# Performance work log

Hardware: AMD Instinct MI355X
Metric: run time of the kernel (lower is better)

The kernel has to match this reference:

```python
import jax, jax.numpy as jnp
import numpy as np

HIDDEN = 2048
FFN = 2048      # ffn_hidden_size (tp_size == 1)
E = 8           # moe_num_experts
TOP_K = 2       # moe_top_k
S = 2048        # number of tokens


def setup_inputs() -> dict:
    key = jax.random.key(0)
    k1, k2, k3, k4 = jax.random.split(key, 4)
    return {
        "hidden_states": jax.random.normal(k1, (S, HIDDEN), jnp.float32),
        "w_qkv": jax.random.normal(k2, (3 * E, HIDDEN), jnp.float32) * 0.02,
        "w1": jax.random.normal(k3, (E, HIDDEN, 2 * FFN), jnp.float32) * 0.02,
        "w2": jax.random.normal(k4, (E, FFN, HIDDEN), jnp.float32) * 0.02,
        "top_k": TOP_K,
    }


def reference(hidden_states, w_qkv, w1, w2, top_k):
    S, H = hidden_states.shape
    # --- ParallelAttention_router (gate), computed in fp32 as in the source ---
    mix = hidden_states @ w_qkv.T                                  # [S, 3E]
    q, k, v = jnp.split(mix.astype(jnp.float32), 3, axis=-1)       # each [S, E]
    # attn_weights[s,i,j] = q[s,i]*k[s,j]; softmax over j; logits = attn @ v
    attn = jax.nn.softmax(q[:, :, None] * k[:, None, :], axis=-1)  # [S, E, E]
    logits = jnp.einsum('sij,sj->si', attn, v)                     # [S, E]
    # --- top-k routing: softmax over selected logits ---
    top_logits, indices = jax.lax.top_k(logits, top_k)             # [S, K]
    scores = jax.nn.softmax(top_logits, axis=-1).astype(hidden_states.dtype)
    # --- experts: per-expert GLU MLP. The torch code sorts tokens by expert and
    # runs a grouped-GEMM loop; mathematically out[s] = sum_k scores[s,k] *
    # MLP_{indices[s,k]}(x[s]). We compute all experts densely (static shapes)
    # and gather/combine, which is the same math. ---
    fc1 = jnp.einsum('sh,ehi->esi', hidden_states, w1)             # [E, S, 2*FFN]
    g, u = jnp.split(fc1, 2, axis=-1)
    inter = jax.nn.silu(g) * u                                     # [E, S, FFN]
    expert_out = jnp.einsum('esi,eih->esh', inter, w2)             # [E, S, H]
    tok = jnp.arange(S)
    out = jnp.zeros_like(hidden_states)
    for kk in range(top_k):  # tiny static loop over top_k (=2)
        out = out + scores[:, kk, None] * expert_out[indices[:, kk], tok]
    return out
```

## Files before the change

kernel.cpp:

```cpp
#include <hip/hip_runtime.h>
#include <math.h>

#define S_TOK 2048
#define HID   2048
#define FFN_  2048
#define NEXP  8
#define NSLOT (S_TOK*2)

typedef short  s8v __attribute__((ext_vector_type(8)));
typedef short  s4v __attribute__((ext_vector_type(4)));
typedef float  f4v __attribute__((ext_vector_type(4)));

__device__ __forceinline__ unsigned short f32_bf16(float f){
  unsigned u = __float_as_uint(f);
  u += 0x7fffu + ((u>>16)&1u);
  return (unsigned short)(u>>16);
}
__device__ __forceinline__ int lds_off(int r,int kq){
  return (r*4 + (kq ^ ((r>>2)&3)))*8;
}

__global__ void init_k(int* hdr){
  if (threadIdx.x < 24) hdr[threadIdx.x] = 0;
}

__global__ __launch_bounds__(256) void convX_k(
    const float* __restrict__ X, unsigned short* __restrict__ Xb)
{
  int i = (blockIdx.x*256 + threadIdx.x)*8;
  f4v a = *reinterpret_cast<const f4v*>(X + i);
  f4v b = *reinterpret_cast<const f4v*>(X + i + 4);
  s8v o;
  o[0]=(short)f32_bf16(a[0]); o[1]=(short)f32_bf16(a[1]);
  o[2]=(short)f32_bf16(a[2]); o[3]=(short)f32_bf16(a[3]);
  o[4]=(short)f32_bf16(b[0]); o[5]=(short)f32_bf16(b[1]);
  o[6]=(short)f32_bf16(b[2]); o[7]=(short)f32_bf16(b[3]);
  *reinterpret_cast<s8v*>(Xb + i) = o;
}

__global__ __launch_bounds__(256) void transp_k(
    const float* __restrict__ src, unsigned short* __restrict__ dst,
    int K, int N)
{
  const int e = blockIdx.z;
  const int n0 = blockIdx.x*64, k0 = blockIdx.y*64;
  src += (size_t)e*K*N;
  dst += (size_t)e*N*K;
  __shared__ __align__(16) unsigned short t[64][72];
  const int tid = threadIdx.x;
  const int r = tid>>2, cq = tid&3;
  #pragma unroll
  for (int i=0;i<4;i++){
    f4v f = *reinterpret_cast<const f4v*>(src + (size_t)(k0+r)*N + n0 + cq*16 + i*4);
    #pragma unroll
    for (int j=0;j<4;j++) t[cq*16+i*4+j][r] = f32_bf16(f[j]);
  }
  __syncthreads();
  #pragma unroll
  for (int i=0;i<2;i++){
    s8v v = *reinterpret_cast<const s8v*>(&t[r][cq*16 + i*8]);
    *reinterpret_cast<s8v*>(dst + (size_t)(n0+r)*K + k0 + cq*16 + i*8) = v;
  }
}

__global__ __launch_bounds__(64) void router_k(
    const float* __restrict__ X, const float* __restrict__ Wqkv,
    int* __restrict__ hdr, int* __restrict__ idx, float* __restrict__ scr)
{
  const int s = blockIdx.x, lane = threadIdx.x;
  const float* x = X + (size_t)s*HID;
  f4v xv[8];
  #pragma unroll
  for (int i=0;i<8;i++) xv[i] = *reinterpret_cast<const f4v*>(x + (i*64+lane)*4);
  float dot[24];
  #pragma unroll
  for (int o=0;o<24;o++){
    const float* w = Wqkv + (size_t)o*HID;
    float a = 0.f;
    #pragma unroll
    for (int i=0;i<8;i++){
      f4v wv = *reinterpret_cast<const f4v*>(w + (i*64+lane)*4);
      a += xv[i][0]*wv[0] + xv[i][1]*wv[1] + xv[i][2]*wv[2] + xv[i][3]*wv[3];
    }
    #pragma unroll
    for (int off=32; off; off>>=1) a += __shfl_xor(a, off, 64);
    dot[o] = a;
  }
  if (lane==0){
    float lg[8];
    #pragma unroll
    for (int i=0;i<8;i++){
      float qi = dot[i];
      float mx = -1e30f;
      #pragma unroll
      for (int j=0;j<8;j++) mx = fmaxf(mx, qi*dot[8+j]);
      float se=0.f, lv=0.f;
      #pragma unroll
      for (int j=0;j<8;j++){
        float e = expf(qi*dot[8+j] - mx);
        se += e; lv += e*dot[16+j];
      }
      lg[i] = lv/se;
    }
    int i0=0; float v0=lg[0];
    #pragma unroll
    for (int i=1;i<8;i++) if (lg[i]>v0){v0=lg[i];i0=i;}
    int i1=-1; float v1=-1e30f;
    #pragma unroll
    for (int i=0;i<8;i++) if (i!=i0 && lg[i]>v1){v1=lg[i];i1=i;}
    float a  = expf(v1-v0);
    float s0 = 1.f/(1.f+a);
    idx[s*2]=i0; idx[s*2+1]=i1;
    scr[s*2]=s0; scr[s*2+1]=a*s0;
    atomicAdd(&hdr[i0],1); atomicAdd(&hdr[i1],1);
  }
}

__global__ void scan_k(int* hdr){
  if (threadIdx.x==0){
    int a=0;
    for (int e=0;e<NEXP;e++){ hdr[16+e]=a; a+=hdr[e]; }
  }
}

__global__ __launch_bounds__(256) void scatter_k(
    const int* __restrict__ idx, const float* __restrict__ scr, int* hdr,
    int* __restrict__ slot_of, int* __restrict__ tok_slot, float* __restrict__ scr_slot)
{
  int s = blockIdx.x*256 + threadIdx.x;
  if (s >= S_TOK) return;
  #pragma unroll
  for (int k=0;k<2;k++){
    int e    = idx[s*2+k];
    int pos  = atomicAdd(&hdr[8+e], 1);
    int slot = hdr[16+e] + pos;
    tok_slot[slot] = s;
    scr_slot[slot] = scr[s*2+k];
    slot_of[s*2+k] = slot;
  }
}

__global__ __launch_bounds__(256,2) void gemm1_k(
    const unsigned short* __restrict__ Xb, const unsigned short* __restrict__ W1t,
    const int* __restrict__ hdr, const int* __restrict__ tok_slot,
    unsigned short* __restrict__ inter)
{
  const int e = blockIdx.z, mt = blockIdx.y, nt = blockIdx.x;
  const int cnt = hdr[e];
  const int m0  = mt*128;
  if (m0 >= cnt) return;
  const int off = hdr[16+e];
  const int n0  = nt*64;
  const unsigned short* W1e = W1t + (size_t)e*(2*FFN_)*HID;

  __shared__ __align__(16) unsigned short sA[128*32];
  __shared__ __align__(16) unsigned short sB[128*32];
  __shared__ int sTok[128];

  const int tid = threadIdx.x;
  if (tid < 128){
    int r = m0 + tid; if (r >= cnt) r = cnt-1;
    sTok[tid] = tok_slot[off + r];
  }
  __syncthreads();

  const int lane = tid & 63, wv = tid >> 6;
  const int wm = wv >> 1, wn = wv & 1;
  const int lm = lane & 15, kq = lane >> 4;
  const int ra = tid >> 2, kg = tid & 3;

  const unsigned short* pA0 = Xb + (size_t)sTok[ra]*HID    + kg*8;
  const unsigned short* pA1 = Xb + (size_t)sTok[ra+64]*HID + kg*8;
  const unsigned short* pB0 = W1e + (size_t)(n0 + ra)*HID        + kg*8;
  const unsigned short* pB1 = W1e + (size_t)(FFN_ + n0 + ra)*HID + kg*8;
  unsigned short* qA0 = &sA[lds_off(ra,    kg)];
  unsigned short* qA1 = &sA[lds_off(ra+64, kg)];
  unsigned short* qB0 = &sB[lds_off(ra,    kg)];
  unsigned short* qB1 = &sB[lds_off(ra+64, kg)];

  f4v zero = {0.f,0.f,0.f,0.f};
  f4v acc[2][2][4];
  #pragma unroll
  for (int a=0;a<2;a++)
    #pragma unroll
    for (int b=0;b<2;b++)
      #pragma unroll
      for (int c=0;c<4;c++) acc[a][b][c]=zero;

  s8v a0 = *reinterpret_cast<const s8v*>(pA0);
  s8v a1 = *reinterpret_cast<const s8v*>(pA1);
  s8v b0 = *reinterpret_cast<const s8v*>(pB0);
  s8v b1 = *reinterpret_cast<const s8v*>(pB1);

  for (int k0=0; k0<HID; k0+=32){
    *reinterpret_cast<s8v*>(qA0) = a0;
    *reinterpret_cast<s8v*>(qA1) = a1;
    *reinterpret_cast<s8v*>(qB0) = b0;
    *reinterpret_cast<s8v*>(qB1) = b1;
    __syncthreads();
    if (k0+32 < HID){
      a0 = *reinterpret_cast<const s8v*>(pA0 + k0+32);
      a1 = *reinterpret_cast<const s8v*>(pA1 + k0+32);
      b0 = *reinterpret_cast<const s8v*>(pB0 + k0+32);
      b1 = *reinterpret_cast<const s8v*>(pB1 + k0+32);
    }
    s8v af[4], bf_[2][2];
    #pragma unroll
    for (int mf=0;mf<4;mf++)
      af[mf] = *reinterpret_cast<const s8v*>(&sA[lds_off(wm*64+mf*16+lm, kq)]);
    #pragma unroll
    for (int st=0; st<2; st++)
      #pragma unroll
      for (int nf=0;nf<2;nf++)
        bf_[st][nf] = *reinterpret_cast<const s8v*>(&sB[lds_off(st*64+wn*32+nf*16+lm, kq)]);
    #pragma unroll
    for (int st=0; st<2; st++)
      #pragma unroll
      for (int nf=0;nf<2;nf++)
        #pragma unroll
        for (int mf=0;mf<4;mf++)
          acc[st][nf][mf] = __builtin_amdgcn_mfma_f32_16x16x32_bf16(
              af[mf], bf_[st][nf], acc[st][nf][mf], 0,0,0);
    __syncthreads();
  }
  const int lq = lane>>4;
  #pragma unroll
  for (int nf=0;nf<2;nf++)
    #pragma unroll
    for (int mf=0;mf<4;mf++){
      f4v g = acc[0][nf][mf], u = acc[1][nf][mf];
      #pragma unroll
      for (int r=0;r<4;r++){
        int row = wm*64 + mf*16 + lq*4 + r;
        if (m0+row < cnt){
          float gv = g[r];
          float val = gv / (1.f + expf(-gv)) * u[r];
          inter[(size_t)(off+m0+row)*FFN_ + n0 + wn*32 + nf*16 + lm] = f32_bf16(val);
        }
      }
    }
}

__global__ __launch_bounds__(256,2) void gemm2_k(
    const unsigned short* __restrict__ inter, const unsigned short* __restrict__ W2t,
    const int* __restrict__ hdr, const float* __restrict__ scr_slot,
    float* __restrict__ eout)
{
  const int e = blockIdx.z, mt = blockIdx.y, nt = blockIdx.x;
  const int cnt = hdr[e];
  const int m0  = mt*128;
  if (m0 >= cnt) return;
  const int off = hdr[16+e];
  const int n0  = nt*128;
  const unsigned short* W2e = W2t + (size_t)e*HID*FFN_;

  __shared__ __align__(16) unsigned short sA[128*32];
  __shared__ __align__(16) unsigned short sB[128*32];
  __shared__ float sScr[128];

  const int tid = threadIdx.x;
  if (tid < 128){
    int r = m0 + tid; if (r >= cnt) r = cnt-1;
    sScr[tid] = scr_slot[off + r];
  }

  const int lane = tid & 63, wv = tid >> 6;
  const int wm = wv >> 1, wn = wv & 1;
  const int lm = lane & 15, kq = lane >> 4;
  const int ra = tid >> 2, kg = tid & 3;

  int r0 = m0 + ra;      if (r0 >= cnt) r0 = cnt-1;
  int r1 = m0 + ra + 64; if (r1 >= cnt) r1 = cnt-1;
  const unsigned short* pA0 = inter + (size_t)(off + r0)*FFN_ + kg*8;
  const unsigned short* pA1 = inter + (size_t)(off + r1)*FFN_ + kg*8;
  const unsigned short* pB0 = W2e + (size_t)(n0 + ra)*FFN_      + kg*8;
  const unsigned short* pB1 = W2e + (size_t)(n0 + ra + 64)*FFN_ + kg*8;
  unsigned short* qA0 = &sA[lds_off(ra,    kg)];
  unsigned short* qA1 = &sA[lds_off(ra+64, kg)];
  unsigned short* qB0 = &sB[lds_off(ra,    kg)];
  unsigned short* qB1 = &sB[lds_off(ra+64, kg)];

  f4v zero = {0.f,0.f,0.f,0.f};
  f4v acc[4][4];
  #pragma unroll
  for (int a=0;a<4;a++)
    #pragma unroll
    for (int b=0;b<4;b++) acc[a][b]=zero;

  s8v a0 = *reinterpret_cast<const s8v*>(pA0);
  s8v a1 = *reinterpret_cast<const s8v*>(pA1);
  s8v b0 = *reinterpret_cast<const s8v*>(pB0);
  s8v b1 = *reinterpret_cast<const s8v*>(pB1);

  for (int k0=0; k0<FFN_; k0+=32){
    *reinterpret_cast<s8v*>(qA0) = a0;
    *reinterpret_cast<s8v*>(qA1) = a1;
    *reinterpret_cast<s8v*>(qB0) = b0;
    *reinterpret_cast<s8v*>(qB1) = b1;
    __syncthreads();
    if (k0+32 < FFN_){
      a0 = *reinterpret_cast<const s8v*>(pA0 + k0+32);
      a1 = *reinterpret_cast<const s8v*>(pA1 + k0+32);
      b0 = *reinterpret_cast<const s8v*>(pB0 + k0+32);
      b1 = *reinterpret_cast<const s8v*>(pB1 + k0+32);
    }
    s8v af[4], bf_[4];
    #pragma unroll
    for (int mf=0;mf<4;mf++)
      af[mf] = *reinterpret_cast<const s8v*>(&sA[lds_off(wm*64+mf*16+lm, kq)]);
    #pragma unroll
    for (int nf=0;nf<4;nf++)
      bf_[nf] = *reinterpret_cast<const s8v*>(&sB[lds_off(wn*64+nf*16+lm, kq)]);
    #pragma unroll
    for (int nf=0;nf<4;nf++)
      #pragma unroll
      for (int mf=0;mf<4;mf++)
        acc[nf][mf] = __builtin_amdgcn_mfma_f32_16x16x32_bf16(
            af[mf], bf_[nf], acc[nf][mf], 0,0,0);
    __syncthreads();
  }
  const int lq = lane>>4;
  #pragma unroll
  for (int nf=0;nf<4;nf++)
    #pragma unroll
    for (int mf=0;mf<4;mf++)
      #pragma unroll
      for (int r=0;r<4;r++){
        int row = wm*64 + mf*16 + lq*4 + r;
        if (m0+row < cnt)
          eout[(size_t)(off+m0+row)*HID + n0 + wn*64 + nf*16 + lm] = acc[nf][mf][r]*sScr[row];
      }
}

__global__ __launch_bounds__(256) void combine_k(
    const float* __restrict__ eout, const int* __restrict__ slot_of,
    float* __restrict__ out)
{
  int s = blockIdx.x, tid = threadIdx.x;
  const float* a = eout + (size_t)slot_of[s*2]  *HID;
  const float* b = eout + (size_t)slot_of[s*2+1]*HID;
  float* o = out + (size_t)s*HID;
  #pragma unroll
  for (int v=tid; v<HID/4; v+=256){
    f4v x = *reinterpret_cast<const f4v*>(a + v*4);
    f4v y = *reinterpret_cast<const f4v*>(b + v*4);
    *reinterpret_cast<f4v*>(o + v*4) = x + y;
  }
}

extern "C" void kernel_launch(void* const* d_in, const int* in_sizes, int n_in,
                              void* d_out, int out_size, void* d_ws, size_t ws_size,
                              hipStream_t stream)
{
  const float* X    = (const float*)d_in[0];
  const float* Wqkv = (const float*)d_in[1];
  const float* W1   = (const float*)d_in[2];
  const float* W2   = (const float*)d_in[3];
  float* out = (float*)d_out;

  char* ws = (char*)d_ws;
  int*   hdr      = (int*)ws;
  int*   idx      = (int*)(ws + 4096);
  float* scr      = (float*)(ws + 4096 + 1*16384);
  int*   slot_of  = (int*)(ws + 4096 + 2*16384);
  int*   tok_slot = (int*)(ws + 4096 + 3*16384);
  float* scr_slot = (float*)(ws + 4096 + 4*16384);
  size_t o = 4096 + 5*16384;
  unsigned short* Xb    = (unsigned short*)(ws + o); o += (size_t)S_TOK*HID*2;
  unsigned short* inter = (unsigned short*)(ws + o); o += (size_t)NSLOT*FFN_*2;
  float*          eout  = (float*)(ws + o);          o += (size_t)NSLOT*HID*4;
  unsigned short* W1t   = (unsigned short*)(ws + o); o += (size_t)NEXP*2*FFN_*HID*2;
  unsigned short* W2t   = (unsigned short*)(ws + o);

  init_k   <<<1,   64, 0, stream>>>(hdr);
  convX_k  <<<(S_TOK*HID/8)/256, 256, 0, stream>>>(X, Xb);
  transp_k <<<dim3((2*FFN_)/64, HID/64, NEXP), 256, 0, stream>>>(W1, W1t, HID, 2*FFN_);
  transp_k <<<dim3(HID/64,     FFN_/64, NEXP), 256, 0, stream>>>(W2, W2t, FFN_, HID);

  router_k <<<S_TOK,64,0, stream>>>(X, Wqkv, hdr, idx, scr);
  scan_k   <<<1,   64, 0, stream>>>(hdr);
  scatter_k<<<(S_TOK+255)/256, 256, 0, stream>>>(idx, scr, hdr, slot_of, tok_slot, scr_slot);
  gemm1_k  <<<dim3(FFN_/64,  S_TOK/128, NEXP), 256, 0, stream>>>(Xb, W1t, hdr, tok_slot, inter);
  gemm2_k  <<<dim3(HID/128,  S_TOK/128, NEXP), 256, 0, stream>>>(inter, W2t, hdr, scr_slot, eout);
  combine_k<<<S_TOK, 256, 0, stream>>>(eout, slot_of, out);
}
```

Baseline: 786.8 us.

## Use direct global-to-LDS loads, fuse combine via atomics, retile weight transpose

Result: no change. 789.3 us (+0.3%).

```diff
diff --git a/kernel.cpp b/kernel.cpp
--- a/kernel.cpp
+++ b/kernel.cpp
@@ -19,9 +19,21 @@
 __device__ __forceinline__ int lds_off(int r,int kq){
   return (r*4 + (kq ^ ((r>>2)&3)))*8;
 }
+__device__ __forceinline__ void gl_lds16(const unsigned short* g, unsigned short* l){
+  __builtin_amdgcn_global_load_lds(
+      (const __attribute__((address_space(1))) unsigned int*)(const void*)g,
+      (__attribute__((address_space(3))) unsigned int*)(void*)l,
+      16, 0, 0);
+}
 
 __global__ void init_k(int* hdr){
   if (threadIdx.x < 24) hdr[threadIdx.x] = 0;
+}
+
+__global__ __launch_bounds__(256) void zero_k(float* __restrict__ p){
+  int i = (blockIdx.x*256 + threadIdx.x)*4;
+  f4v z = {0.f,0.f,0.f,0.f};
+  *reinterpret_cast<f4v*>(p + i) = z;
 }
 
 __global__ __launch_bounds__(256) void convX_k(
@@ -43,23 +55,32 @@
     int K, int N)
 {
   const int e = blockIdx.z;
-  const int n0 = blockIdx.x*64, k0 = blockIdx.y*64;
-  src += (size_t)e*K*N;
-  dst += (size_t)e*N*K;
-  __shared__ __align__(16) unsigned short t[64][72];
+  const int k0 = blockIdx.y*64, n0 = blockIdx.x*128;
+  src += (size_t)e*K*N + (size_t)k0*N + n0;
+  dst += (size_t)e*N*K + (size_t)n0*K + k0;
+  __shared__ __align__(16) unsigned short t[128*66];
   const int tid = threadIdx.x;
-  const int r = tid>>2, cq = tid&3;
-  #pragma unroll
-  for (int i=0;i<4;i++){
-    f4v f = *reinterpret_cast<const f4v*>(src + (size_t)(k0+r)*N + n0 + cq*16 + i*4);
-    #pragma unroll
-    for (int j=0;j<4;j++) t[cq*16+i*4+j][r] = f32_bf16(f[j]);
+  const int nb = tid & 31;
+  const int kb = tid >> 5;
+  f4v f[8];
+  #pragma unroll
+  for (int j=0;j<8;j++)
+    f[j] = *reinterpret_cast<const f4v*>(src + (size_t)(kb*8+j)*N + nb*4);
+  #pragma unroll
+  for (int c=0;c<4;c++){
+    int n = nb*4 + c;
+    s8v v;
+    #pragma unroll
+    for (int j=0;j<8;j++) v[j] = (short)f32_bf16(f[j][c]);
+    *reinterpret_cast<s8v*>(&t[n*66 + ((kb ^ ((n>>5)&3))*8)]) = v;
   }
   __syncthreads();
   #pragma unroll
-  for (int i=0;i<2;i++){
-    s8v v = *reinterpret_cast<const s8v*>(&t[r][cq*16 + i*8]);
-    *reinterpret_cast<s8v*>(dst + (size_t)(n0+r)*K + k0 + cq*16 + i*8) = v;
+  for (int p=0;p<4;p++){
+    int n = p*32 + (tid>>3);
+    int c = tid & 7;
+    s8v v = *reinterpret_cast<const s8v*>(&t[n*66 + ((c ^ ((n>>5)&3))*8)]);
+    *reinterpret_cast<s8v*>(dst + (size_t)n*K + c*8) = v;
   }
 }
 
@@ -125,7 +146,7 @@
 
 __global__ __launch_bounds__(256) void scatter_k(
     const int* __restrict__ idx, const float* __restrict__ scr, int* hdr,
-    int* __restrict__ slot_of, int* __restrict__ tok_slot, float* __restrict__ scr_slot)
+    int* __restrict__ tok_slot, float* __restrict__ scr_slot)
 {
   int s = blockIdx.x*256 + threadIdx.x;
   if (s >= S_TOK) return;
@@ -136,11 +157,10 @@
     int slot = hdr[16+e] + pos;
     tok_slot[slot] = s;
     scr_slot[slot] = scr[s*2+k];
-    slot_of[s*2+k] = slot;
-  }
-}
-
-__global__ __launch_bounds__(256,2) void gemm1_k(
+  }
+}
+
+__global__ __launch_bounds__(256,3) void gemm1_k(
     const unsigned short* __restrict__ Xb, const unsigned short* __restrict__ W1t,
     const int* __restrict__ hdr, const int* __restrict__ tok_slot,
     unsigned short* __restrict__ inter)
@@ -167,16 +187,17 @@
   const int lane = tid & 63, wv = tid >> 6;
   const int wm = wv >> 1, wn = wv & 1;
   const int lm = lane & 15, kq = lane >> 4;
-  const int ra = tid >> 2, kg = tid & 3;
-
-  const unsigned short* pA0 = Xb + (size_t)sTok[ra]*HID    + kg*8;
-  const unsigned short* pA1 = Xb + (size_t)sTok[ra+64]*HID + kg*8;
-  const unsigned short* pB0 = W1e + (size_t)(n0 + ra)*HID        + kg*8;
-  const unsigned short* pB1 = W1e + (size_t)(FFN_ + n0 + ra)*HID + kg*8;
-  unsigned short* qA0 = &sA[lds_off(ra,    kg)];
-  unsigned short* qA1 = &sA[lds_off(ra+64, kg)];
-  unsigned short* qB0 = &sB[lds_off(ra,    kg)];
-  unsigned short* qB1 = &sB[lds_off(ra+64, kg)];
+  const int srow = lane >> 2, kg = lane & 3;
+  const int kgs  = kg ^ (srow >> 2);
+
+  const unsigned short* gA0 = Xb + (size_t)sTok[wv*16 + srow]*HID      + kgs*8;
+  const unsigned short* gA1 = Xb + (size_t)sTok[64 + wv*16 + srow]*HID + kgs*8;
+  const unsigned short* gB0 = W1e + (size_t)(n0 + wv*16 + srow)*HID        + kgs*8;
+  const unsigned short* gB1 = W1e + (size_t)(FFN_ + n0 + wv*16 + srow)*HID + kgs*8;
+  unsigned short* lA0 = sA + (wv*16)*32;
+  unsigned short* lA1 = sA + (64 + wv*16)*32;
+  unsigned short* lB0 = sB + (wv*16)*32;
+  unsigned short* lB1 = sB + (64 + wv*16)*32;
 
   f4v zero = {0.f,0.f,0.f,0.f};
   f4v acc[2][2][4];
@@ -187,24 +208,12 @@
       #pragma unroll
       for (int c=0;c<4;c++) acc[a][b][c]=zero;
 
-  s8v a0 = *reinterpret_cast<const s8v*>(pA0);
-  s8v a1 = *reinterpret_cast<const s8v*>(pA1);
-  s8v b0 = *reinterpret_cast<const s8v*>(pB0);
-  s8v b1 = *reinterpret_cast<const s8v*>(pB1);
-
   for (int k0=0; k0<HID; k0+=32){
-    *reinterpret_cast<s8v*>(qA0) = a0;
-    *reinterpret_cast<s8v*>(qA1) = a1;
-    *reinterpret_cast<s8v*>(qB0) = b0;
-    *reinterpret_cast<s8v*>(qB1) = b1;
+    gl_lds16(gA0, lA0); gl_lds16(gA1, lA1);
+    gl_lds16(gB0, lB0); gl_lds16(gB1, lB1);
+    gA0 += 32; gA1 += 32; gB0 += 32; gB1 += 32;
     __syncthreads();
-    if (k0+32 < HID){
-      a0 = *reinterpret_cast<const s8v*>(pA0 + k0+32);
-      a1 = *reinterpret_cast<const s8v*>(pA1 + k0+32);
-      b0 = *reinterpret_cast<const s8v*>(pB0 + k0+32);
-      b1 = *reinterpret_cast<const s8v*>(pB1 + k0+32);
-    }
-    s8v af[4], bf_[2][2];
+    s8v af[4], bfr[2][2];
     #pragma unroll
     for (int mf=0;mf<4;mf++)
       af[mf] = *reinterpret_cast<const s8v*>(&sA[lds_off(wm*64+mf*16+lm, kq)]);
@@ -212,7 +221,7 @@
     for (int st=0; st<2; st++)
       #pragma unroll
       for (int nf=0;nf<2;nf++)
-        bf_[st][nf] = *reinterpret_cast<const s8v*>(&sB[lds_off(st*64+wn*32+nf*16+lm, kq)]);
+        bfr[st][nf] = *reinterpret_cast<const s8v*>(&sB[lds_off(st*64+wn*32+nf*16+lm, kq)]);
     #pragma unroll
     for (int st=0; st<2; st++)
       #pragma unroll
@@ -220,7 +229,7 @@
         #pragma unroll
         for (int mf=0;mf<4;mf++)
           acc[st][nf][mf] = __builtin_amdgcn_mfma_f32_16x16x32_bf16(
-              af[mf], bf_[st][nf], acc[st][nf][mf], 0,0,0);
+              af[mf], bfr[st][nf], acc[st][nf][mf], 0,0,0);
     __syncthreads();
   }
   const int lq = lane>>4;
@@ -241,10 +250,10 @@
     }
 }
 
-__global__ __launch_bounds__(256,2) void gemm2_k(
+__global__ __launch_bounds__(256,3) void gemm2_k(
     const unsigned short* __restrict__ inter, const unsigned short* __restrict__ W2t,
-    const int* __restrict__ hdr, const float* __restrict__ scr_slot,
-    float* __restrict__ eout)
+    const int* __restrict__ hdr, const int* __restrict__ tok_slot,
+    const float* __restrict__ scr_slot, float* __restrict__ out)
 {
   const int e = blockIdx.z, mt = blockIdx.y, nt = blockIdx.x;
   const int cnt = hdr[e];
@@ -256,29 +265,32 @@
 
   __shared__ __align__(16) unsigned short sA[128*32];
   __shared__ __align__(16) unsigned short sB[128*32];
+  __shared__ int   sTok[128];
   __shared__ float sScr[128];
 
   const int tid = threadIdx.x;
   if (tid < 128){
     int r = m0 + tid; if (r >= cnt) r = cnt-1;
+    sTok[tid] = tok_slot[off + r];
     sScr[tid] = scr_slot[off + r];
   }
 
   const int lane = tid & 63, wv = tid >> 6;
   const int wm = wv >> 1, wn = wv & 1;
   const int lm = lane & 15, kq = lane >> 4;
-  const int ra = tid >> 2, kg = tid & 3;
-
-  int r0 = m0 + ra;      if (r0 >= cnt) r0 = cnt-1;
-  int r1 = m0 + ra + 64; if (r1 >= cnt) r1 = cnt-1;
-  const unsigned short* pA0 = inter + (size_t)(off + r0)*FFN_ + kg*8;
-  const unsigned short* pA1 = inter + (size_t)(off + r1)*FFN_ + kg*8;
-  const unsigned short* pB0 = W2e + (size_t)(n0 + ra)*FFN_      + kg*8;
-  const unsigned short* pB1 = W2e + (size_t)(n0 + ra + 64)*FFN_ + kg*8;
-  unsigned short* qA0 = &sA[lds_off(ra,    kg)];
-  unsigned short* qA1 = &sA[lds_off(ra+64, kg)];
-  unsigned short* qB0 = &sB[lds_off(ra,    kg)];
-  unsigned short* qB1 = &sB[lds_off(ra+64, kg)];
+  const int srow = lane >> 2, kg = lane & 3;
+  const int kgs  = kg ^ (srow >> 2);
+
+  int r0 = m0 + wv*16 + srow;      if (r0 >= cnt) r0 = cnt-1;
+  int r1 = m0 + 64 + wv*16 + srow; if (r1 >= cnt) r1 = cnt-1;
+  const unsigned short* gA0 = inter + (size_t)(off + r0)*FFN_ + kgs*8;
+  const unsigned short* gA1 = inter + (size_t)(off + r1)*FFN_ + kgs*8;
+  const unsigned short* gB0 = W2e + (size_t)(n0 + wv*16 + srow)*FFN_      + kgs*8;
+  const unsigned short* gB1 = W2e + (size_t)(n0 + 64 + wv*16 + srow)*FFN_ + kgs*8;
+  unsigned short* lA0 = sA + (wv*16)*32;
+  unsigned short* lA1 = sA + (64 + wv*16)*32;
+  unsigned short* lB0 = sB + (wv*16)*32;
+  unsigned short* lB1 = sB + (64 + wv*16)*32;
 
   f4v zero = {0.f,0.f,0.f,0.f};
   f4v acc[4][4];
@@ -287,36 +299,26 @@
     #pragma unroll
     for (int b=0;b<4;b++) acc[a][b]=zero;
 
-  s8v a0 = *reinterpret_cast<const s8v*>(pA0);
-  s8v a1 = *reinterpret_cast<const s8v*>(pA1);
-  s8v b0 = *reinterpret_cast<const s8v*>(pB0);
-  s8v b1 = *reinterpret_cast<const s8v*>(pB1);
+  __syncthreads();
 
   for (int k0=0; k0<FFN_; k0+=32){
-    *reinterpret_cast<s8v*>(qA0) = a0;
-    *reinterpret_cast<s8v*>(qA1) = a1;
-    *reinterpret_cast<s8v*>(qB0) = b0;
-    *reinterpret_cast<s8v*>(qB1) = b1;
+    gl_lds16(gA0, lA0); gl_lds16(gA1, lA1);
+    gl_lds16(gB0, lB0); gl_lds16(gB1, lB1);
+    gA0 += 32; gA1 += 32; gB0 += 32; gB1 += 32;
     __syncthreads();
-    if (k0+32 < FFN_){
-      a0 = *reinterpret_cast<const s8v*>(pA0 + k0+32);
-      a1 = *reinterpret_cast<const s8v*>(pA1 + k0+32);
-      b0 = *reinterpret_cast<const s8v*>(pB0 + k0+32);
-      b1 = *reinterpret_cast<const s8v*>(pB1 + k0+32);
-    }
-    s8v af[4], bf_[4];
+    s8v af[4], bfr[4];
     #pragma unroll
     for (int mf=0;mf<4;mf++)
       af[mf] = *reinterpret_cast<const s8v*>(&sA[lds_off(wm*64+mf*16+lm, kq)]);
     #pragma unroll
     for (int nf=0;nf<4;nf++)
-      bf_[nf] = *reinterpret_cast<const s8v*>(&sB[lds_off(wn*64+nf*16+lm, kq)]);
+      bfr[nf] = *reinterpret_cast<const s8v*>(&sB[lds_off(wn*64+nf*16+lm, kq)]);
     #pragma unroll
     for (int nf=0;nf<4;nf++)
       #pragma unroll
       for (int mf=0;mf<4;mf++)
         acc[nf][mf] = __builtin_amdgcn_mfma_f32_16x16x32_bf16(
-            af[mf], bf_[nf], acc[nf][mf], 0,0,0);
+            af[mf], bfr[nf], acc[nf][mf], 0,0,0);
     __syncthreads();
   }
   const int lq = lane>>4;
@@ -328,24 +330,9 @@
       for (int r=0;r<4;r++){
         int row = wm*64 + mf*16 + lq*4 + r;
         if (m0+row < cnt)
-          eout[(size_t)(off+m0+row)*HID + n0 + wn*64 + nf*16 + lm] = acc[nf][mf][r]*sScr[row];
+          atomicAdd(&out[(size_t)sTok[row]*HID + n0 + wn*64 + nf*16 + lm],
+                    acc[nf][mf][r]*sScr[row]);
       }
-}
-
-__global__ __launch_bounds__(256) void combine_k(
-    const float* __restrict__ eout, const int* __restrict__ slot_of,
-    float* __restrict__ out)
-{
-  int s = blockIdx.x, tid = threadIdx.x;
-  const float* a = eout + (size_t)slot_of[s*2]  *HID;
-  const float* b = eout + (size_t)slot_of[s*2+1]*HID;
-  float* o = out + (size_t)s*HID;
-  #pragma unroll
-  for (int v=tid; v<HID/4; v+=256){
-    f4v x = *reinterpret_cast<const f4v*>(a + v*4);
-    f4v y = *reinterpret_cast<const f4v*>(b + v*4);
-    *reinterpret_cast<f4v*>(o + v*4) = x + y;
-  }
 }
 
 extern "C" void kernel_launch(void* const* d_in, const int* in_sizes, int n_in,
@@ -362,25 +349,23 @@
   int*   hdr      = (int*)ws;
   int*   idx      = (int*)(ws + 4096);
   float* scr      = (float*)(ws + 4096 + 1*16384);
-  int*   slot_of  = (int*)(ws + 4096 + 2*16384);
-  int*   tok_slot = (int*)(ws + 4096 + 3*16384);
-  float* scr_slot = (float*)(ws + 4096 + 4*16384);
-  size_t o = 4096 + 5*16384;
+  int*   tok_slot = (int*)(ws + 4096 + 2*16384);
+  float* scr_slot = (float*)(ws + 4096 + 3*16384);
+  size_t o = 4096 + 4*16384;
   unsigned short* Xb    = (unsigned short*)(ws + o); o += (size_t)S_TOK*HID*2;
   unsigned short* inter = (unsigned short*)(ws + o); o += (size_t)NSLOT*FFN_*2;
-  float*          eout  = (float*)(ws + o);          o += (size_t)NSLOT*HID*4;
   unsigned short* W1t   = (unsigned short*)(ws + o); o += (size_t)NEXP*2*FFN_*HID*2;
   unsigned short* W2t   = (unsigned short*)(ws + o);
 
   init_k   <<<1,   64, 0, stream>>>(hdr);
+  zero_k   <<<(S_TOK*HID/4)/256, 256, 0, stream>>>(out);
   convX_k  <<<(S_TOK*HID/8)/256, 256, 0, stream>>>(X, Xb);
-  transp_k <<<dim3((2*FFN_)/64, HID/64, NEXP), 256, 0, stream>>>(W1, W1t, HID, 2*FFN_);
-  transp_k <<<dim3(HID/64,     FFN_/64, NEXP), 256, 0, stream>>>(W2, W2t, FFN_, HID);
+  transp_k <<<dim3((2*FFN_)/128, HID/64, NEXP), 256, 0, stream>>>(W1, W1t, HID, 2*FFN_);
+  transp_k <<<dim3(HID/128,     FFN_/64, NEXP), 256, 0, stream>>>(W2, W2t, FFN_, HID);
 
   router_k <<<S_TOK,64,0, stream>>>(X, Wqkv, hdr, idx, scr);
   scan_k   <<<1,   64, 0, stream>>>(hdr);
-  scatter_k<<<(S_TOK+255)/256, 256, 0, stream>>>(idx, scr, hdr, slot_of, tok_slot, scr_slot);
+  scatter_k<<<(S_TOK+255)/256, 256, 0, stream>>>(idx, scr, hdr, tok_slot, scr_slot);
   gemm1_k  <<<dim3(FFN_/64,  S_TOK/128, NEXP), 256, 0, stream>>>(Xb, W1t, hdr, tok_slot, inter);
-  gemm2_k  <<<dim3(HID/128,  S_TOK/128, NEXP), 256, 0, stream>>>(inter, W2t, hdr, scr_slot, eout);
-  combine_k<<<S_TOK, 256, 0, stream>>>(eout, slot_of, out);
-}
+  gemm2_k  <<<dim3(HID/128,  S_TOK/128, NEXP), 256, 0, stream>>>(inter, W2t, hdr, tok_slot, scr_slot, out);
+}
```
